# Optimization experiments

Hardware: AMD Instinct MI355X
Metric: run time of the kernel (lower is better)

Reference implementation:

```python
import jax, jax.numpy as jnp
import numpy as np

EPS = 1e-05
B, I, N, O = 1024, 256, 1024, 256

def setup_inputs() -> dict:
    key = jax.random.key(0)
    ks = jax.random.split(key, 6)
    return {
        "x_re": jax.random.normal(ks[0], (B, I, 1), dtype=jnp.float32),
        "x_im": jax.random.normal(ks[1], (B, I, 1), dtype=jnp.float32),
        "G_re": jax.random.normal(ks[2], (I, N), dtype=jnp.float32) / np.sqrt(I).astype(np.float32),
        "G_im": jax.random.normal(ks[3], (I, N), dtype=jnp.float32) / np.sqrt(I).astype(np.float32),
        "s_re": jnp.ones((1, N), dtype=jnp.float32),
        "s_im": jnp.ones((1, N), dtype=jnp.float32),
        "W_re": jax.random.normal(ks[4], (N, O), dtype=jnp.float32) * np.float32(np.sqrt(5 * np.exp(2) * I / (12 * N * O))),
        "W_im": jax.random.normal(ks[5], (N, O), dtype=jnp.float32) * np.float32(np.sqrt(5 * np.exp(2) * I / (12 * N * O))),
        "b_re": jnp.zeros((1, O), dtype=jnp.float32),
        "b_im": jnp.zeros((1, O), dtype=jnp.float32),
    }

def reference(x_re, x_im, G_re, G_im, s_re, s_im, W_re, W_im, b_re, b_im):
    # (B, inputs, 1) - (inputs, neurons) -> (B, inputs, neurons); reduce over inputs
    v_re = jnp.sum((x_re - G_re) ** 2, axis=1, keepdims=True)  # (B, 1, N)
    v_im = jnp.sum((x_im - G_im) ** 2, axis=1, keepdims=True)  # (B, 1, N)
    phi_re = jnp.exp(-v_re / jnp.maximum(s_re, EPS))  # (B, 1, N)
    phi_im = jnp.exp(-v_im / jnp.maximum(s_im, EPS))  # (B, 1, N)
    # complex matmul (phi_re + i phi_im) @ (W_re + i W_im) + (b_re + i b_im)
    y_re = jnp.matmul(phi_re, W_re) - jnp.matmul(phi_im, W_im) + b_re  # (B, 1, O)
    y_im = jnp.matmul(phi_re, W_im) + jnp.matmul(phi_im, W_re) + b_im  # (B, 1, O)
    return jnp.stack([y_re, y_im], axis=-1)  # (B, 1, O, 2) = real/imag
```

## Files before the change

kernel.cpp:

```cpp
#include <hip/hip_runtime.h>
#include <math.h>

#define B_ 1024
#define I_ 256
#define N_ 1024
#define O_ 256
#define EPSV 1e-5f

typedef unsigned short u16;
typedef short bf16x8 __attribute__((ext_vector_type(8)));
typedef float f32x4 __attribute__((ext_vector_type(4)));
typedef int i32x4 __attribute__((ext_vector_type(4)));

__device__ inline u16 f2bf(float f) {
    union { float f; unsigned int u; } v; v.f = f;
    unsigned int r = v.u + 0x7FFFu + ((v.u >> 16) & 1u);
    return (u16)(r >> 16);
}


__device__ inline void transconv_frag(const float* __restrict__ in,
                                      u16* __restrict__ out, int R, int C,
                                      int r0, int c0, int t, float (*tile)[69]) {
    const int lr = t >> 2, lq = t & 3;
    #pragma unroll
    for (int j = 0; j < 4; ++j) {
        float4 v = *(const float4*)(in + (size_t)(r0 + lr) * C + c0 + lq * 16 + j * 4);
        *(float4*)&tile[lr][lq * 16 + j * 4] = v;
    }
    __syncthreads();
    const int oc = t >> 2, oq = t & 3;
    const int row = c0 + oc;
    const int ktiles = R >> 5;
    #pragma unroll
    for (int h = 0; h < 2; ++h) {
        const int k0 = r0 + oq * 16 + h * 8;
        const int kt = k0 >> 5, quad = (k0 >> 3) & 3;
        __align__(16) u16 tmp[8];
        #pragma unroll
        for (int e = 0; e < 8; ++e)
            tmp[e] = f2bf(tile[oq * 16 + h * 8 + e][oc]);
        const size_t off = ((size_t)((row >> 4) * ktiles + kt)) * 512
                         + (quad * 16 + (row & 15)) * 8;
        *(int4*)(out + off) = *(const int4*)tmp;
    }
}

__global__ __launch_bounds__(256) void prep_kernel(
    const float* __restrict__ x_re, const float* __restrict__ x_im,
    const float* __restrict__ G_re, const float* __restrict__ G_im,
    const float* __restrict__ W_re, const float* __restrict__ W_im,
    u16* __restrict__ Xfr, u16* __restrict__ Xfi,
    u16* __restrict__ GTfr, u16* __restrict__ GTfi,
    u16* __restrict__ WTfr, u16* __restrict__ WTfi,
    float* __restrict__ xsq_re, float* __restrict__ xsq_im,
    float* __restrict__ gsq_re, float* __restrict__ gsq_im)
{
    __shared__ float smem[64][69];
    const int blk = blockIdx.x, t = threadIdx.x;

    if (blk < 256) {
        const int w = t >> 6, l = t & 63;
        const int row = blk * 4 + w;
        float4 a = *((const float4*)(x_re + (size_t)row * I_) + l);
        float4 c = *((const float4*)(x_im + (size_t)row * I_) + l);
        float sr = a.x*a.x + a.y*a.y + a.z*a.z + a.w*a.w;
        float si = c.x*c.x + c.y*c.y + c.z*c.z + c.w*c.w;
        #pragma unroll
        for (int off = 32; off > 0; off >>= 1) {
            sr += __shfl_down(sr, off);
            si += __shfl_down(si, off);
        }
        if (l == 0) { xsq_re[row] = sr; xsq_im[row] = si; }
    } else if (blk < 272) {
        const int l = t & 63, w = t >> 6;
        const int n = (blk - 256) * 64 + l;
        float sr = 0.f, si = 0.f;
        for (int i = w * 64; i < w * 64 + 64; ++i) {
            float g = G_re[(size_t)i * N_ + n]; sr += g * g;
            float h = G_im[(size_t)i * N_ + n]; si += h * h;
        }
        float (*red)[64] = (float(*)[64])smem;
        red[w][l] = sr; red[4 + w][l] = si;
        __syncthreads();
        if (w == 0) {
            gsq_re[n] = red[0][l] + red[1][l] + red[2][l] + red[3][l];
            gsq_im[n] = red[4][l] + red[5][l] + red[6][l] + red[7][l];
        }
    } else if (blk < 528) {
        const int tile_lin = (blk - 272) * 4 + (t >> 6);
        const int comp = tile_lin >> 9;
        const int tl = tile_lin & 511;
        const int mt = tl >> 3, kt = tl & 7;
        const int lane = t & 63;
        const int quad = lane & 3, l16 = lane >> 2;
        const float* src = (comp ? x_im : x_re)
                         + (size_t)(mt * 16 + l16) * I_ + kt * 32 + quad * 8;
        float4 a0 = *(const float4*)src;
        float4 a1 = *(const float4*)(src + 4);
        __align__(16) u16 tmp[8];
        tmp[0] = f2bf(a0.x); tmp[1] = f2bf(a0.y); tmp[2] = f2bf(a0.z); tmp[3] = f2bf(a0.w);
        tmp[4] = f2bf(a1.x); tmp[5] = f2bf(a1.y); tmp[6] = f2bf(a1.z); tmp[7] = f2bf(a1.w);
        u16* dst = (comp ? Xfi : Xfr)
                 + (size_t)(mt * 8 + kt) * 512 + (quad * 16 + l16) * 8;
        *(int4*)dst = *(const int4*)tmp;
    } else if (blk < 656) {
        const int local = blk - 528;
        const int comp = local >> 6, rem = local & 63;
        const int rt = rem >> 4, ct = rem & 15;
        transconv_frag(comp ? G_im : G_re, comp ? GTfi : GTfr,
                       I_, N_, rt * 64, ct * 64, t, smem);
    } else {
        const int local = blk - 656;
        const int comp = local >> 6, rem = local & 63;
        const int rt = rem >> 2, ct = rem & 3;
        transconv_frag(comp ? W_im : W_re, comp ? WTfi : WTfr,
                       N_, O_, rt * 64, ct * 64, t, smem);
    }
}

__global__ __launch_bounds__(256) void phi_mfma(
    const u16* __restrict__ Xfr, const u16* __restrict__ Xfi,
    const u16* __restrict__ GTfr, const u16* __restrict__ GTfi,
    const float* __restrict__ xsq_re, const float* __restrict__ xsq_im,
    const float* __restrict__ gsq_re, const float* __restrict__ gsq_im,
    const float* __restrict__ s_re, const float* __restrict__ s_im,
    u16* __restrict__ Pfr, u16* __restrict__ Pfi)
{
    __shared__ u16 pbuf[8 * 512];
    const int z = blockIdx.z;
    const u16* Xf  = z ? Xfi : Xfr;
    const u16* GTf = z ? GTfi : GTfr;
    const float* xsq = z ? xsq_im : xsq_re;
    const float* gsq = z ? gsq_im : gsq_re;
    const float* s   = z ? s_im : s_re;
    u16* Pf = z ? Pfi : Pfr;

    const int t = threadIdx.x;
    const int w = t >> 6, lane = t & 63;
    const int quad = lane >> 4, l16 = lane & 15;
    const int mw = (w >> 1) * 32, nw = (w & 1) * 32;
    const int mt0 = blockIdx.y * 4 + (mw >> 4);
    const int nt0 = blockIdx.x * 4 + (nw >> 4);

    const u16* Ab = Xf  + lane * 8;
    const u16* Bb = GTf + lane * 8;

    f32x4 acc[2][2] = {};
    #pragma unroll
    for (int kt = 0; kt < 8; ++kt) {
        bf16x8 a0 = *(const bf16x8*)(Ab + (size_t)(mt0 * 8 + kt) * 512);
        bf16x8 a1 = *(const bf16x8*)(Ab + (size_t)((mt0 + 1) * 8 + kt) * 512);
        bf16x8 b0 = *(const bf16x8*)(Bb + (size_t)(nt0 * 8 + kt) * 512);
        bf16x8 b1 = *(const bf16x8*)(Bb + (size_t)((nt0 + 1) * 8 + kt) * 512);
        acc[0][0] = __builtin_amdgcn_mfma_f32_16x16x32_bf16(a0, b0, acc[0][0], 0, 0, 0);
        acc[0][1] = __builtin_amdgcn_mfma_f32_16x16x32_bf16(a0, b1, acc[0][1], 0, 0, 0);
        acc[1][0] = __builtin_amdgcn_mfma_f32_16x16x32_bf16(a1, b0, acc[1][0], 0, 0, 0);
        acc[1][1] = __builtin_amdgcn_mfma_f32_16x16x32_bf16(a1, b1, acc[1][1], 0, 0, 0);
    }

    const int m0 = blockIdx.y * 64, n0 = blockIdx.x * 64;
    #pragma unroll
    for (int mt = 0; mt < 2; ++mt)
        #pragma unroll
        for (int nt = 0; nt < 2; ++nt) {
            const int col = nw + nt * 16 + l16;
            const float gq = gsq[n0 + col];
            const float inv_s = 1.0f / fmaxf(s[n0 + col], EPSV);
            #pragma unroll
            for (int r = 0; r < 4; ++r) {
                const int row = mw + mt * 16 + quad * 4 + r;
                const float v = xsq[m0 + row] - 2.0f * acc[mt][nt][r] + gq;
                const u16 p = f2bf(__expf(-v * inv_s));
                const int lt = (row >> 4) * 2 + (col >> 5);
                pbuf[lt * 512 + (((col >> 3) & 3) * 16 + (row & 15)) * 8 + (col & 7)] = p;
            }
        }
    __syncthreads();

    const int lt = t >> 5, s32 = t & 31;
    const int mt_g = blockIdx.y * 4 + (lt >> 1);
    const int kt_g = blockIdx.x * 2 + (lt & 1);
    const u16* src = pbuf + lt * 512 + s32 * 16;
    u16* dst = Pf + (size_t)(mt_g * 32 + kt_g) * 512 + s32 * 16;
    *(int4*)dst = *(const int4*)src;
    *((int4*)dst + 1) = *((const int4*)src + 1);
}

__global__ __launch_bounds__(256) void y_mfma(
    const u16* __restrict__ Pfr, const u16* __restrict__ Pfi,
    const u16* __restrict__ WTfr, const u16* __restrict__ WTfi,
    const float* __restrict__ b_re, const float* __restrict__ b_im,
    float* __restrict__ out)
{
    __shared__ float red[4][2][32][33];
    const int t = threadIdx.x;
    const int w = t >> 6, lane = t & 63;
    const int quad = lane >> 4, l16 = lane & 15;
    const int pm0 = blockIdx.y * 2;
    const int wo0 = blockIdx.x * 2;

    const u16* Ar = Pfr + lane * 8;
    const u16* Ai = Pfi + lane * 8;
    const u16* Br = WTfr + lane * 8;
    const u16* Bi = WTfi + lane * 8;

    f32x4 cr[2][2] = {}, ci[2][2] = {};
    #pragma unroll
    for (int ks = 0; ks < 8; ++ks) {
        const int kt = w * 8 + ks;
        bf16x8 ar[2], ai[2], an[2], br[2], bi[2];
        #pragma unroll
        for (int mt = 0; mt < 2; ++mt) {
            ar[mt] = *(const bf16x8*)(Ar + (size_t)((pm0 + mt) * 32 + kt) * 512);
            ai[mt] = *(const bf16x8*)(Ai + (size_t)((pm0 + mt) * 32 + kt) * 512);
            i32x4 tv = (*(const i32x4*)&ai[mt]) ^ 0x80008000;
            an[mt] = *(const bf16x8*)&tv;
        }
        #pragma unroll
        for (int nt = 0; nt < 2; ++nt) {
            br[nt] = *(const bf16x8*)(Br + (size_t)((wo0 + nt) * 32 + kt) * 512);
            bi[nt] = *(const bf16x8*)(Bi + (size_t)((wo0 + nt) * 32 + kt) * 512);
        }
        #pragma unroll
        for (int mt = 0; mt < 2; ++mt)
            #pragma unroll
            for (int nt = 0; nt < 2; ++nt) {
                cr[mt][nt] = __builtin_amdgcn_mfma_f32_16x16x32_bf16(
                    ar[mt], br[nt], cr[mt][nt], 0, 0, 0);
                cr[mt][nt] = __builtin_amdgcn_mfma_f32_16x16x32_bf16(
                    an[mt], bi[nt], cr[mt][nt], 0, 0, 0);
                ci[mt][nt] = __builtin_amdgcn_mfma_f32_16x16x32_bf16(
                    ar[mt], bi[nt], ci[mt][nt], 0, 0, 0);
                ci[mt][nt] = __builtin_amdgcn_mfma_f32_16x16x32_bf16(
                    ai[mt], br[nt], ci[mt][nt], 0, 0, 0);
            }
    }

    #pragma unroll
    for (int mt = 0; mt < 2; ++mt)
        #pragma unroll
        for (int nt = 0; nt < 2; ++nt) {
            const int o = nt * 16 + l16;
            #pragma unroll
            for (int r = 0; r < 4; ++r) {
                const int b = mt * 16 + quad * 4 + r;
                red[w][0][b][o] = cr[mt][nt][r];
                red[w][1][b][o] = ci[mt][nt][r];
            }
        }
    __syncthreads();

    const int b = t >> 3, og = (t & 7) * 4;
    const int gb = blockIdx.y * 32 + b;
    #pragma unroll
    for (int p = 0; p < 2; ++p) {
        const int o = og + p * 2;
        const int go = blockIdx.x * 32 + o;
        float r0 = red[0][0][b][o]   + red[1][0][b][o]   + red[2][0][b][o]   + red[3][0][b][o];
        float i0 = red[0][1][b][o]   + red[1][1][b][o]   + red[2][1][b][o]   + red[3][1][b][o];
        float r1 = red[0][0][b][o+1] + red[1][0][b][o+1] + red[2][0][b][o+1] + red[3][0][b][o+1];
        float i1 = red[0][1][b][o+1] + red[1][1][b][o+1] + red[2][1][b][o+1] + red[3][1][b][o+1];
        float4 v;
        v.x = r0 + b_re[go];     v.y = i0 + b_im[go];
        v.z = r1 + b_re[go + 1]; v.w = i1 + b_im[go + 1];
        *(float4*)(out + ((size_t)gb * O_ + go) * 2) = v;
    }
}

extern "C" void kernel_launch(void* const* d_in, const int* in_sizes, int n_in,
                              void* d_out, int out_size, void* d_ws, size_t ws_size,
                              hipStream_t stream) {
    const float* x_re = (const float*)d_in[0];
    const float* x_im = (const float*)d_in[1];
    const float* G_re = (const float*)d_in[2];
    const float* G_im = (const float*)d_in[3];
    const float* s_re = (const float*)d_in[4];
    const float* s_im = (const float*)d_in[5];
    const float* W_re = (const float*)d_in[6];
    const float* W_im = (const float*)d_in[7];
    const float* b_re = (const float*)d_in[8];
    const float* b_im = (const float*)d_in[9];
    float* out = (float*)d_out;

    u16* Xfr  = (u16*)d_ws;
    u16* Xfi  = Xfr  + (size_t)B_ * I_;
    u16* GTfr = Xfi  + (size_t)B_ * I_;
    u16* GTfi = GTfr + (size_t)N_ * I_;
    u16* WTfr = GTfi + (size_t)N_ * I_;
    u16* WTfi = WTfr + (size_t)O_ * N_;
    u16* Pfr  = WTfi + (size_t)O_ * N_;
    u16* Pfi  = Pfr  + (size_t)B_ * N_;
    float* xsq_re = (float*)(Pfi + (size_t)B_ * N_);
    float* xsq_im = xsq_re + B_;
    float* gsq_re = xsq_im + B_;
    float* gsq_im = gsq_re + N_;

    prep_kernel<<<784, 256, 0, stream>>>(
        x_re, x_im, G_re, G_im, W_re, W_im,
        Xfr, Xfi, GTfr, GTfi, WTfr, WTfi,
        xsq_re, xsq_im, gsq_re, gsq_im);

    phi_mfma<<<dim3(N_ / 64, B_ / 64, 2), 256, 0, stream>>>(
        Xfr, Xfi, GTfr, GTfi, xsq_re, xsq_im, gsq_re, gsq_im,
        s_re, s_im, Pfr, Pfi);

    y_mfma<<<dim3(O_ / 32, B_ / 32), 256, 0, stream>>>(
        Pfr, Pfi, WTfr, WTfi, b_re, b_im, out);
}
```

Measured before the change: 100.2 us.

## Prefetch next k-slice in both MFMA loops and halve y_mfma row tile

Both MFMA kernels now software-pipeline their fragment loads, fetching the next k-step's A and B fragments while the current step's MFMAs issue, so global load latency overlaps with compute. The y_mfma kernel also shrinks its batch tile from 32 to 16 rows per block, doubling the grid to raise occupancy and parallelism, with a smaller shared reduction buffer. The cost is more redundant loads of W fragments across blocks and extra registers for the prefetched fragments.

```diff
diff --git a/kernel.cpp b/kernel.cpp
--- a/kernel.cpp
+++ b/kernel.cpp
@@ -145,18 +145,32 @@
 
     const u16* Ab = Xf  + lane * 8;
     const u16* Bb = GTf + lane * 8;
+    const size_t a0o = (size_t)(mt0 * 8) * 512;
+    const size_t a1o = (size_t)((mt0 + 1) * 8) * 512;
+    const size_t b0o = (size_t)(nt0 * 8) * 512;
+    const size_t b1o = (size_t)((nt0 + 1) * 8) * 512;
+
+    bf16x8 cA0 = *(const bf16x8*)(Ab + a0o);
+    bf16x8 cA1 = *(const bf16x8*)(Ab + a1o);
+    bf16x8 cB0 = *(const bf16x8*)(Bb + b0o);
+    bf16x8 cB1 = *(const bf16x8*)(Bb + b1o);
 
     f32x4 acc[2][2] = {};
     #pragma unroll
     for (int kt = 0; kt < 8; ++kt) {
-        bf16x8 a0 = *(const bf16x8*)(Ab + (size_t)(mt0 * 8 + kt) * 512);
-        bf16x8 a1 = *(const bf16x8*)(Ab + (size_t)((mt0 + 1) * 8 + kt) * 512);
-        bf16x8 b0 = *(const bf16x8*)(Bb + (size_t)(nt0 * 8 + kt) * 512);
-        bf16x8 b1 = *(const bf16x8*)(Bb + (size_t)((nt0 + 1) * 8 + kt) * 512);
-        acc[0][0] = __builtin_amdgcn_mfma_f32_16x16x32_bf16(a0, b0, acc[0][0], 0, 0, 0);
-        acc[0][1] = __builtin_amdgcn_mfma_f32_16x16x32_bf16(a0, b1, acc[0][1], 0, 0, 0);
-        acc[1][0] = __builtin_amdgcn_mfma_f32_16x16x32_bf16(a1, b0, acc[1][0], 0, 0, 0);
-        acc[1][1] = __builtin_amdgcn_mfma_f32_16x16x32_bf16(a1, b1, acc[1][1], 0, 0, 0);
+        bf16x8 nA0, nA1, nB0, nB1;
+        if (kt < 7) {
+            const size_t ko = (size_t)(kt + 1) * 512;
+            nA0 = *(const bf16x8*)(Ab + a0o + ko);
+            nA1 = *(const bf16x8*)(Ab + a1o + ko);
+            nB0 = *(const bf16x8*)(Bb + b0o + ko);
+            nB1 = *(const bf16x8*)(Bb + b1o + ko);
+        }
+        acc[0][0] = __builtin_amdgcn_mfma_f32_16x16x32_bf16(cA0, cB0, acc[0][0], 0, 0, 0);
+        acc[0][1] = __builtin_amdgcn_mfma_f32_16x16x32_bf16(cA0, cB1, acc[0][1], 0, 0, 0);
+        acc[1][0] = __builtin_amdgcn_mfma_f32_16x16x32_bf16(cA1, cB0, acc[1][0], 0, 0, 0);
+        acc[1][1] = __builtin_amdgcn_mfma_f32_16x16x32_bf16(cA1, cB1, acc[1][1], 0, 0, 0);
+        cA0 = nA0; cA1 = nA1; cB0 = nB0; cB1 = nB1;
     }
 
     const int m0 = blockIdx.y * 64, n0 = blockIdx.x * 64;
@@ -193,79 +207,79 @@
     const float* __restrict__ b_re, const float* __restrict__ b_im,
     float* __restrict__ out)
 {
-    __shared__ float red[4][2][32][33];
+    __shared__ float red[4][2][16][34];
     const int t = threadIdx.x;
     const int w = t >> 6, lane = t & 63;
     const int quad = lane >> 4, l16 = lane & 15;
-    const int pm0 = blockIdx.y * 2;
+    const int pm = blockIdx.y;
     const int wo0 = blockIdx.x * 2;
 
     const u16* Ar = Pfr + lane * 8;
     const u16* Ai = Pfi + lane * 8;
     const u16* Br = WTfr + lane * 8;
     const u16* Bi = WTfi + lane * 8;
-
-    f32x4 cr[2][2] = {}, ci[2][2] = {};
+    const size_t ao = (size_t)(pm * 32 + w * 8) * 512;
+    const size_t b0o = (size_t)(wo0 * 32 + w * 8) * 512;
+    const size_t b1o = (size_t)((wo0 + 1) * 32 + w * 8) * 512;
+
+    bf16x8 cAr = *(const bf16x8*)(Ar + ao);
+    bf16x8 cAi = *(const bf16x8*)(Ai + ao);
+    bf16x8 cBr0 = *(const bf16x8*)(Br + b0o);
+    bf16x8 cBi0 = *(const bf16x8*)(Bi + b0o);
+    bf16x8 cBr1 = *(const bf16x8*)(Br + b1o);
+    bf16x8 cBi1 = *(const bf16x8*)(Bi + b1o);
+
+    f32x4 cr[2] = {}, ci[2] = {};
     #pragma unroll
     for (int ks = 0; ks < 8; ++ks) {
-        const int kt = w * 8 + ks;
-        bf16x8 ar[2], ai[2], an[2], br[2], bi[2];
+        bf16x8 nAr, nAi, nBr0, nBi0, nBr1, nBi1;
+        if (ks < 7) {
+            const size_t ko = (size_t)(ks + 1) * 512;
+            nAr  = *(const bf16x8*)(Ar + ao + ko);
+            nAi  = *(const bf16x8*)(Ai + ao + ko);
+            nBr0 = *(const bf16x8*)(Br + b0o + ko);
+            nBi0 = *(const bf16x8*)(Bi + b0o + ko);
+            nBr1 = *(const bf16x8*)(Br + b1o + ko);
+            nBi1 = *(const bf16x8*)(Bi + b1o + ko);
+        }
+        i32x4 tv = (*(const i32x4*)&cAi) ^ 0x80008000;
+        bf16x8 cAn = *(const bf16x8*)&tv;
+        cr[0] = __builtin_amdgcn_mfma_f32_16x16x32_bf16(cAr, cBr0, cr[0], 0, 0, 0);
+        cr[0] = __builtin_amdgcn_mfma_f32_16x16x32_bf16(cAn, cBi0, cr[0], 0, 0, 0);
+        ci[0] = __builtin_amdgcn_mfma_f32_16x16x32_bf16(cAr, cBi0, ci[0], 0, 0, 0);
+        ci[0] = __builtin_amdgcn_mfma_f32_16x16x32_bf16(cAi, cBr0, ci[0], 0, 0, 0);
+        cr[1] = __builtin_amdgcn_mfma_f32_16x16x32_bf16(cAr, cBr1, cr[1], 0, 0, 0);
+        cr[1] = __builtin_amdgcn_mfma_f32_16x16x32_bf16(cAn, cBi1, cr[1], 0, 0, 0);
+        ci[1] = __builtin_amdgcn_mfma_f32_16x16x32_bf16(cAr, cBi1, ci[1], 0, 0, 0);
+        ci[1] = __builtin_amdgcn_mfma_f32_16x16x32_bf16(cAi, cBr1, ci[1], 0, 0, 0);
+        cAr = nAr; cAi = nAi;
+        cBr0 = nBr0; cBi0 = nBi0; cBr1 = nBr1; cBi1 = nBi1;
+    }
+
+    #pragma unroll
+    for (int nt = 0; nt < 2; ++nt) {
+        const int o = nt * 16 + l16;
         #pragma unroll
-        for (int mt = 0; mt < 2; ++mt) {
-            ar[mt] = *(const bf16x8*)(Ar + (size_t)((pm0 + mt) * 32 + kt) * 512);
-            ai[mt] = *(const bf16x8*)(Ai + (size_t)((pm0 + mt) * 32 + kt) * 512);
-            i32x4 tv = (*(const i32x4*)&ai[mt]) ^ 0x80008000;
-            an[mt] = *(const bf16x8*)&tv;
-        }
-        #pragma unroll
-        for (int nt = 0; nt < 2; ++nt) {
-            br[nt] = *(const bf16x8*)(Br + (size_t)((wo0 + nt) * 32 + kt) * 512);
-            bi[nt] = *(const bf16x8*)(Bi + (size_t)((wo0 + nt) * 32 + kt) * 512);
-        }
-        #pragma unroll
-        for (int mt = 0; mt < 2; ++mt)
-            #pragma unroll
-            for (int nt = 0; nt < 2; ++nt) {
-                cr[mt][nt] = __builtin_amdgcn_mfma_f32_16x16x32_bf16(
-                    ar[mt], br[nt], cr[mt][nt], 0, 0, 0);
-                cr[mt][nt] = __builtin_amdgcn_mfma_f32_16x16x32_bf16(
-                    an[mt], bi[nt], cr[mt][nt], 0, 0, 0);
-                ci[mt][nt] = __builtin_amdgcn_mfma_f32_16x16x32_bf16(
-                    ar[mt], bi[nt], ci[mt][nt], 0, 0, 0);
-                ci[mt][nt] = __builtin_amdgcn_mfma_f32_16x16x32_bf16(
-                    ai[mt], br[nt], ci[mt][nt], 0, 0, 0);
-            }
-    }
-
-    #pragma unroll
-    for (int mt = 0; mt < 2; ++mt)
-        #pragma unroll
-        for (int nt = 0; nt < 2; ++nt) {
-            const int o = nt * 16 + l16;
-            #pragma unroll
-            for (int r = 0; r < 4; ++r) {
-                const int b = mt * 16 + quad * 4 + r;
-                red[w][0][b][o] = cr[mt][nt][r];
-                red[w][1][b][o] = ci[mt][nt][r];
-            }
-        }
+        for (int r = 0; r < 4; ++r) {
+            const int b = quad * 4 + r;
+            red[w][0][b][o] = cr[nt][r];
+            red[w][1][b][o] = ci[nt][r];
+        }
+    }
     __syncthreads();
 
-    const int b = t >> 3, og = (t & 7) * 4;
-    const int gb = blockIdx.y * 32 + b;
-    #pragma unroll
-    for (int p = 0; p < 2; ++p) {
-        const int o = og + p * 2;
-        const int go = blockIdx.x * 32 + o;
-        float r0 = red[0][0][b][o]   + red[1][0][b][o]   + red[2][0][b][o]   + red[3][0][b][o];
-        float i0 = red[0][1][b][o]   + red[1][1][b][o]   + red[2][1][b][o]   + red[3][1][b][o];
-        float r1 = red[0][0][b][o+1] + red[1][0][b][o+1] + red[2][0][b][o+1] + red[3][0][b][o+1];
-        float i1 = red[0][1][b][o+1] + red[1][1][b][o+1] + red[2][1][b][o+1] + red[3][1][b][o+1];
-        float4 v;
-        v.x = r0 + b_re[go];     v.y = i0 + b_im[go];
-        v.z = r1 + b_re[go + 1]; v.w = i1 + b_im[go + 1];
-        *(float4*)(out + ((size_t)gb * O_ + go) * 2) = v;
-    }
+    const int b = t >> 4, oq = t & 15;
+    const int o = oq * 2;
+    const int gb = blockIdx.y * 16 + b;
+    const int go = blockIdx.x * 32 + o;
+    float r0 = red[0][0][b][o]   + red[1][0][b][o]   + red[2][0][b][o]   + red[3][0][b][o];
+    float i0 = red[0][1][b][o]   + red[1][1][b][o]   + red[2][1][b][o]   + red[3][1][b][o];
+    float r1 = red[0][0][b][o+1] + red[1][0][b][o+1] + red[2][0][b][o+1] + red[3][0][b][o+1];
+    float i1 = red[0][1][b][o+1] + red[1][1][b][o+1] + red[2][1][b][o+1] + red[3][1][b][o+1];
+    float4 v;
+    v.x = r0 + b_re[go];     v.y = i0 + b_im[go];
+    v.z = r1 + b_re[go + 1]; v.w = i1 + b_im[go + 1];
+    *(float4*)(out + ((size_t)gb * O_ + go) * 2) = v;
 }
 
 extern "C" void kernel_launch(void* const* d_in, const int* in_sizes, int n_in,
@@ -305,6 +319,6 @@
         Xfr, Xfi, GTfr, GTfi, xsq_re, xsq_im, gsq_re, gsq_im,
         s_re, s_im, Pfr, Pfi);
 
-    y_mfma<<<dim3(O_ / 32, B_ / 32), 256, 0, stream>>>(
+    y_mfma<<<dim3(O_ / 32, B_ / 16), 256, 0, stream>>>(
         Pfr, Pfi, WTfr, WTfi, b_re, b_im, out);
 }
```

Result: faster. 95.75 us (-4.4%).
